# Performance work log

Hardware: AMD Instinct MI355X
Metric: run time of the kernel (lower is better)

The kernel has to match this reference:

```python
import jax, jax.numpy as jnp
import numpy as np

N_DRUG = 20000
N_DIS = 40000
E = 500000
D_IN = 128
D_OUT = 128
SLOPE = 0.01  # F.leaky_relu default negative_slope


def setup_inputs() -> dict:
    key = jax.random.key(0)
    ks = jax.random.split(key, 17)
    s = 1.0 / np.sqrt(D_IN)
    inp = {
        'feat_drug': jax.random.normal(ks[0], (N_DRUG, D_IN), jnp.float32),
        'feat_disease': jax.random.normal(ks[1], (N_DIS, D_IN), jnp.float32),
        'src_ind': jax.random.randint(ks[2], (E,), 0, N_DRUG, jnp.int32),
        'dst_ind': jax.random.randint(ks[3], (E,), 0, N_DIS, jnp.int32),
        'src_rev': jax.random.randint(ks[4], (E,), 0, N_DIS, jnp.int32),
        'dst_rev': jax.random.randint(ks[5], (E,), 0, N_DRUG, jnp.int32),
        'src_dd': jax.random.randint(ks[6], (E,), 0, N_DIS, jnp.int32),
        'dst_dd': jax.random.randint(ks[7], (E,), 0, N_DIS, jnp.int32),
        'W_ind': jax.random.normal(ks[8], (D_IN, D_OUT), jnp.float32) * s,
        'b_ind': jax.random.normal(ks[9], (D_OUT,), jnp.float32) * s,
        'W_rev': jax.random.normal(ks[10], (D_IN, D_OUT), jnp.float32) * s,
        'b_rev': jax.random.normal(ks[11], (D_OUT,), jnp.float32) * s,
        'W_dd': jax.random.normal(ks[12], (D_IN, D_OUT), jnp.float32) * s,
        'b_dd': jax.random.normal(ks[13], (D_OUT,), jnp.float32) * s,
        'a_ind': jax.random.normal(ks[14], (2 * D_OUT,), jnp.float32) * s,
        'a_rev': jax.random.normal(ks[15], (2 * D_OUT,), jnp.float32) * s,
        'a_dd': jax.random.normal(ks[16], (2 * D_OUT,), jnp.float32) * s,
    }
    return inp


def _leaky(x):
    return jnp.where(x >= 0, x, SLOPE * x)


def _etype_softmax_agg(wh_src, wh_dst, src, dst, a, n_dst):
    # per-edge message gather
    m = wh_src[src]                      # [E, D_OUT]
    wd = wh_dst[dst]                     # [E, D_OUT]
    # attn_fc(concat(m, wd)) == m @ a[:D] + wd @ a[D:]
    e = _leaky(m @ a[:D_OUT] + wd @ a[D_OUT:])   # [E]
    # segment softmax over dst (per-node mailbox softmax)
    emax = jax.ops.segment_max(e, dst, num_segments=n_dst)
    ex = jnp.exp(e - emax[dst])
    denom = jax.ops.segment_sum(ex, dst, num_segments=n_dst)
    alpha = ex / denom[dst]
    # weighted scatter-sum aggregation
    return jax.ops.segment_sum(alpha[:, None] * m, dst, num_segments=n_dst)


def reference(feat_drug, feat_disease, src_ind, dst_ind, src_rev, dst_rev,
              src_dd, dst_dd, W_ind, b_ind, W_rev, b_rev, W_dd, b_dd,
              a_ind, a_rev, a_dd):
    # per-etype linear projections of the source node type
    Wh_ind = feat_drug @ W_ind + b_ind       # drug nodes, etype 'indication'
    Wh_rev = feat_disease @ W_rev + b_rev    # disease nodes, etype 'rev_indication'
    Wh_dd = feat_disease @ W_dd + b_dd       # disease nodes, etype 'dd' (self type)
    # indication: drug->disease pairs with dst key Wh_rev_indication
    h_dis = _etype_softmax_agg(Wh_ind, Wh_rev, src_ind, dst_ind, a_ind, N_DIS)
    # dd: same src/dst type, uses Wh_dd on both sides; cross-etype 'sum' reducer
    h_dis = h_dis + _etype_softmax_agg(Wh_dd, Wh_dd, src_dd, dst_dd, a_dd, N_DIS)
    # rev_indication: disease->drug pairs with dst key Wh_indication
    h_drug = _etype_softmax_agg(Wh_rev, Wh_ind, src_rev, dst_rev, a_rev, N_DRUG)
    return (h_drug, h_dis)
```

## Files before the change

kernel.cpp:

```cpp
#include <hip/hip_runtime.h>
#include <hip/hip_bf16.h>

#define N_DRUG 20000
#define N_DIS  40000
#define NE     500000
#define D      128
#define PITCH  136
#define NTOT   100000
#define NQ     (NE / 4)
#define NQ3    (3 * NQ)
#define CSTR   16
#define WSZ    (128 * PITCH)
#define BIN    64

typedef __hip_bfloat16 bf16;
typedef __attribute__((ext_vector_type(8))) short short8;
typedef __attribute__((ext_vector_type(4))) float floatx4;

__device__ __forceinline__ float b2f(bf16 x) { return __bfloat162float(x); }

#define GB_DRUG 313
#define GB_DIS  625
#define GB_ALL  (GB_DRUG + 2 * GB_DIS)
#define GH      ((NQ3 + 255) / 256)

__global__ void k_prep(const float* __restrict__ W_ind, const float* __restrict__ W_rev,
                       const float* __restrict__ W_dd, bf16* __restrict__ WbfT)
{
    const int et = blockIdx.x >> 4;
    const int sl = blockIdx.x & 15;
    const float* W = (et == 0) ? W_ind : (et == 1) ? W_rev : W_dd;
    bf16* out = WbfT + (size_t)et * WSZ;
    int idx = sl * 1024 + threadIdx.x;
#pragma unroll
    for (int r = 0; r < 4; ++r, idx += 256) {
        int k = idx >> 7, n = idx & 127;
        out[n * PITCH + k] = __float2bfloat16(W[idx]);
    }
}

__global__ void k_gh(const float* __restrict__ feat_drug, const float* __restrict__ feat_dis,
                     const bf16* __restrict__ WbfT,
                     const float* __restrict__ b_ind, const float* __restrict__ b_rev,
                     const float* __restrict__ b_dd,
                     const float* __restrict__ a_ind, const float* __restrict__ a_rev,
                     const float* __restrict__ a_dd,
                     bf16* __restrict__ Wh_ind, bf16* __restrict__ Wh_rev,
                     bf16* __restrict__ Wh_dd,
                     float* __restrict__ s_src_ind, float* __restrict__ s_dst_rev,
                     float* __restrict__ s_src_rev, float* __restrict__ s_dst_ind,
                     float* __restrict__ s_src_dd,  float* __restrict__ s_dst_dd,
                     const int4* __restrict__ se_ind, const int4* __restrict__ d_ind,
                     const int4* __restrict__ se_dd,  const int4* __restrict__ d_dd,
                     const int4* __restrict__ se_rev, const int4* __restrict__ d_rev,
                     int* __restrict__ cnt, unsigned short* __restrict__ col)
{
    __shared__ __align__(16) bf16 WT[128 * PITCH];
    __shared__ __align__(16) bf16 FS[64 * PITCH];
    const int tid = threadIdx.x;
    const int blk = blockIdx.x;

    int gemm_blk;
    if (blk < 2 * GH) {
        if (blk & 1) {
            const int i = (blk >> 1) * 256 + tid;
            if (i >= NQ3) return;
            int4 d, s; int boff;
            if (i < NQ)          { d = d_ind[i];              s = se_ind[i];          boff = 0; }
            else if (i < 2 * NQ) { int j = i - NQ;     d = d_dd[j];  s = se_dd[j];  boff = 40000; }
            else                 { int j = i - 2 * NQ; d = d_rev[j]; s = se_rev[j]; boff = 80000; }
            int x0 = boff + d.x, x1 = boff + d.y, x2 = boff + d.z, x3 = boff + d.w;
            int r0 = atomicAdd(&cnt[x0 * CSTR], 1);
            if (r0 < BIN) col[(size_t)x0 * BIN + r0] = (unsigned short)s.x;
            int r1 = atomicAdd(&cnt[x1 * CSTR], 1);
            if (r1 < BIN) col[(size_t)x1 * BIN + r1] = (unsigned short)s.y;
            int r2 = atomicAdd(&cnt[x2 * CSTR], 1);
            if (r2 < BIN) col[(size_t)x2 * BIN + r2] = (unsigned short)s.z;
            int r3 = atomicAdd(&cnt[x3 * CSTR], 1);
            if (r3 < BIN) col[(size_t)x3 * BIN + r3] = (unsigned short)s.w;
            return;
        }
        gemm_blk = blk >> 1;
    } else {
        gemm_blk = GH + (blk - 2 * GH);
    }

    const float *feat, *bias, *a1, *a2;
    const bf16* Wt;
    bf16* Wh; float *s1, *s2;
    int M, row0;
    if (gemm_blk < GB_DRUG) {
        feat = feat_drug; M = N_DRUG; row0 = gemm_blk * 64;
        Wt = WbfT; bias = b_ind; a1 = a_ind; a2 = a_rev + D;
        Wh = Wh_ind; s1 = s_src_ind; s2 = s_dst_rev;
    } else if (gemm_blk < GB_DRUG + GB_DIS) {
        feat = feat_dis; M = N_DIS; row0 = (gemm_blk - GB_DRUG) * 64;
        Wt = WbfT + WSZ; bias = b_rev; a1 = a_rev; a2 = a_ind + D;
        Wh = Wh_rev; s1 = s_src_rev; s2 = s_dst_ind;
    } else {
        feat = feat_dis; M = N_DIS; row0 = (gemm_blk - GB_DRUG - GB_DIS) * 64;
        Wt = WbfT + 2 * WSZ; bias = b_dd; a1 = a_dd; a2 = a_dd + D;
        Wh = Wh_dd; s1 = s_src_dd; s2 = s_dst_dd;
    }

#pragma unroll
    for (int rep = 0; rep < 9; ++rep) {
        int off = rep * 2048 + tid * 8;
        if (off < WSZ)
            *(short8*)(WT + off) = *(const short8*)(Wt + off);
    }
#pragma unroll
    for (int rep = 0; rep < 8; ++rep) {
        int idx = rep * 1024 + tid * 4;
        int r = idx >> 7, k = idx & 127;
        int gr = row0 + r;
        float4 f4 = (gr < M) ? *(const float4*)(feat + (size_t)gr * D + k)
                             : make_float4(0.f, 0.f, 0.f, 0.f);
        FS[r * PITCH + k + 0] = __float2bfloat16(f4.x);
        FS[r * PITCH + k + 1] = __float2bfloat16(f4.y);
        FS[r * PITCH + k + 2] = __float2bfloat16(f4.z);
        FS[r * PITCH + k + 3] = __float2bfloat16(f4.w);
    }
    __syncthreads();

    const int wave = tid >> 6;
    const int lane = tid & 63;
    const int m0   = wave * 16;
    const int arow = lane & 15;
    const int kq   = lane >> 4;

    floatx4 acc[8];
#pragma unroll
    for (int t = 0; t < 8; ++t) acc[t] = (floatx4){0.f, 0.f, 0.f, 0.f};

#pragma unroll
    for (int ks = 0; ks < 4; ++ks) {
        const int kb = ks * 32 + kq * 8;
        short8 afrag = *(const short8*)(FS + (m0 + arow) * PITCH + kb);
#pragma unroll
        for (int t = 0; t < 8; ++t) {
            short8 bfrag = *(const short8*)(WT + (t * 16 + arow) * PITCH + kb);
            acc[t] = __builtin_amdgcn_mfma_f32_16x16x32_bf16(afrag, bfrag, acc[t], 0, 0, 0);
        }
    }

    const int crow = m0 + kq * 4;
    float p1[4] = {0.f, 0.f, 0.f, 0.f};
    float p2[4] = {0.f, 0.f, 0.f, 0.f};
#pragma unroll
    for (int t = 0; t < 8; ++t) {
        const int n = t * 16 + arow;
        const float bn = bias[n], a1n = a1[n], a2n = a2[n];
#pragma unroll
        for (int r = 0; r < 4; ++r) {
            float v = acc[t][r] + bn;
            int gr = row0 + crow + r;
            if (gr < M) Wh[(size_t)gr * D + n] = __float2bfloat16(v);
            p1[r] += v * a1n;
            p2[r] += v * a2n;
        }
    }
#pragma unroll
    for (int r = 0; r < 4; ++r) {
#pragma unroll
        for (int off = 1; off < 16; off <<= 1) {
            p1[r] += __shfl_xor(p1[r], off);
            p2[r] += __shfl_xor(p2[r], off);
        }
    }
    if (arow == 0) {
#pragma unroll
        for (int r = 0; r < 4; ++r) {
            int gr = row0 + crow + r;
            if (gr < M) { s1[gr] = p1[r]; s2[gr] = p2[r]; }
        }
    }
}

__device__ __forceinline__ float2 agg_seg(int b, int c, const unsigned short* __restrict__ col,
                                          const float* __restrict__ ssrc, float sdv,
                                          const bf16* __restrict__ Whs, int lane)
{
    float ax = 0.f, ay = 0.f, dpart = 0.f;
    for (int t0 = 0; t0 < c; t0 += 64) {
        const int rem = c - t0;
        const int k = rem < 64 ? rem : 64;
        int myc = 0; float myex = 0.f;
        if (lane < k) {
            myc = col[b + t0 + lane];
            float e = ssrc[myc] + sdv;
            e = (e >= 0.f) ? e : 0.01f * e;
            myex = __expf(fminf(e, 30.f));
        }
        dpart += myex;
        const int kk = (k + 7) & ~7;
        for (int j = 0; j < kk; j += 8) {
            int sv[8]; float ev[8]; __hip_bfloat162 w[8];
#pragma unroll
            for (int u = 0; u < 8; ++u) {
                sv[u] = __shfl(myc, j + u);
                ev[u] = __shfl(myex, j + u);
            }
#pragma unroll
            for (int u = 0; u < 8; ++u)
                w[u] = *(const __hip_bfloat162*)(Whs + (size_t)sv[u] * D + 2 * lane);
#pragma unroll
            for (int u = 0; u < 8; ++u) {
                ax += ev[u] * b2f(w[u].x);
                ay += ev[u] * b2f(w[u].y);
            }
        }
    }
    float denom = dpart;
#pragma unroll
    for (int off = 32; off; off >>= 1) denom += __shfl_xor(denom, off);
    const float inv = (c > 0) ? 1.f / denom : 0.f;
    return make_float2(ax * inv, ay * inv);
}

__global__ void k_agg(const int* __restrict__ cnt, const unsigned short* __restrict__ col,
                      const float* __restrict__ ss_ind, const float* __restrict__ sd_ind,
                      const bf16* __restrict__ Wh_ind,
                      const float* __restrict__ ss_dd, const float* __restrict__ sd_dd,
                      const bf16* __restrict__ Wh_dd,
                      const float* __restrict__ ss_rev, const float* __restrict__ sd_rev,
                      const bf16* __restrict__ Wh_rev,
                      float* __restrict__ out_dis, float* __restrict__ out_drug)
{
    const int g    = (int)((blockIdx.x * blockDim.x + threadIdx.x) >> 6);
    const int lane = threadIdx.x & 63;
    if (g < N_DIS) {
        float2 r1 = agg_seg(g * BIN, cnt[g * CSTR], col,
                            ss_ind, sd_ind[g], Wh_ind, lane);
        float2 r2 = agg_seg((40000 + g) * BIN, cnt[(40000 + g) * CSTR], col,
                            ss_dd, sd_dd[g], Wh_dd, lane);
        *(float2*)(out_dis + (size_t)g * D + 2 * lane) = make_float2(r1.x + r2.x, r1.y + r2.y);
    } else if (g < N_DIS + N_DRUG) {
        const int gg = g - N_DIS;
        float2 r = agg_seg((80000 + gg) * BIN, cnt[(80000 + gg) * CSTR], col,
                           ss_rev, sd_rev[gg], Wh_rev, lane);
        *(float2*)(out_drug + (size_t)gg * D + 2 * lane) = r;
    }
}

extern "C" void kernel_launch(void* const* d_in, const int* in_sizes, int n_in,
                              void* d_out, int out_size, void* d_ws, size_t ws_size,
                              hipStream_t stream)
{
    const float* feat_drug = (const float*)d_in[0];
    const float* feat_dis  = (const float*)d_in[1];
    const int*   src_ind   = (const int*)d_in[2];
    const int*   dst_ind   = (const int*)d_in[3];
    const int*   src_rev   = (const int*)d_in[4];
    const int*   dst_rev   = (const int*)d_in[5];
    const int*   src_dd    = (const int*)d_in[6];
    const int*   dst_dd    = (const int*)d_in[7];
    const float* W_ind     = (const float*)d_in[8];
    const float* b_ind     = (const float*)d_in[9];
    const float* W_rev     = (const float*)d_in[10];
    const float* b_rev     = (const float*)d_in[11];
    const float* W_dd      = (const float*)d_in[12];
    const float* b_dd      = (const float*)d_in[13];
    const float* a_ind     = (const float*)d_in[14];
    const float* a_rev     = (const float*)d_in[15];
    const float* a_dd      = (const float*)d_in[16];

    float* out_drug = (float*)d_out;
    float* out_dis  = (float*)d_out + (size_t)N_DRUG * D;

    char* ws = (char*)d_ws;
    size_t off = 0;
    auto alloc = [&](size_t bytes) -> void* {
        void* p = ws + off;
        off += (bytes + 255) & ~(size_t)255;
        return p;
    };

    bf16* Wh_ind = (bf16*)alloc(sizeof(bf16) * (size_t)N_DRUG * D);
    bf16* Wh_rev = (bf16*)alloc(sizeof(bf16) * (size_t)N_DIS * D);
    bf16* Wh_dd  = (bf16*)alloc(sizeof(bf16) * (size_t)N_DIS * D);
    bf16* WbfT   = (bf16*)alloc(sizeof(bf16) * 3 * WSZ);

    float* s_src_ind = (float*)alloc(sizeof(float) * N_DRUG);
    float* s_dst_rev = (float*)alloc(sizeof(float) * N_DRUG);
    float* s_src_rev = (float*)alloc(sizeof(float) * N_DIS);
    float* s_dst_ind = (float*)alloc(sizeof(float) * N_DIS);
    float* s_src_dd  = (float*)alloc(sizeof(float) * N_DIS);
    float* s_dst_dd  = (float*)alloc(sizeof(float) * N_DIS);

    unsigned short* col = (unsigned short*)alloc(sizeof(unsigned short) * (size_t)NTOT * BIN);

    const size_t nzero = (size_t)NTOT * CSTR;
    int* cnt = (int*)alloc(sizeof(int) * nzero);

    hipMemsetAsync(cnt, 0, sizeof(int) * nzero, stream);

    k_prep<<<48, 256, 0, stream>>>(W_ind, W_rev, W_dd, WbfT);

    k_gh<<<GB_ALL + GH, 256, 0, stream>>>(
        feat_drug, feat_dis, WbfT, b_ind, b_rev, b_dd,
        a_ind, a_rev, a_dd, Wh_ind, Wh_rev, Wh_dd,
        s_src_ind, s_dst_rev, s_src_rev, s_dst_ind, s_src_dd, s_dst_dd,
        (const int4*)src_ind, (const int4*)dst_ind,
        (const int4*)src_dd,  (const int4*)dst_dd,
        (const int4*)src_rev, (const int4*)dst_rev,
        cnt, col);

    k_agg<<<(N_DIS + N_DRUG + 3) / 4, 256, 0, stream>>>(cnt, col,
                                                        s_src_ind, s_dst_ind, Wh_ind,
                                                        s_src_dd, s_dst_dd, Wh_dd,
                                                        s_src_rev, s_dst_rev, Wh_rev,
                                                        out_dis, out_drug);
}
```

Baseline: 234.8 us.

## Fuse memset into prep kernel and interleave two disease segment aggregations

Replaces the separate hipMemsetAsync with zeroing done by extra blocks inside the weight-prep kernel, removing one launch. In the aggregation kernel, the indication and dd segments for each disease node are now processed together in one loop, issuing both sets of gathered row loads before accumulating, so more memory requests are in flight per wavefront. Counts are clamped to BIN, which also guards against overflowing the column bins. This costs more registers per thread, which may lower occupancy.

```diff
diff --git a/kernel.cpp b/kernel.cpp
--- a/kernel.cpp
+++ b/kernel.cpp
@@ -12,6 +12,7 @@
 #define CSTR   16
 #define WSZ    (128 * PITCH)
 #define BIN    64
+#define NZERO4 ((NTOT * CSTR) / 4)
 
 typedef __hip_bfloat16 bf16;
 typedef __attribute__((ext_vector_type(8))) short short8;
@@ -24,18 +25,26 @@
 #define GB_ALL  (GB_DRUG + 2 * GB_DIS)
 #define GH      ((NQ3 + 255) / 256)
 
-__global__ void k_prep(const float* __restrict__ W_ind, const float* __restrict__ W_rev,
-                       const float* __restrict__ W_dd, bf16* __restrict__ WbfT)
-{
-    const int et = blockIdx.x >> 4;
-    const int sl = blockIdx.x & 15;
-    const float* W = (et == 0) ? W_ind : (et == 1) ? W_rev : W_dd;
-    bf16* out = WbfT + (size_t)et * WSZ;
-    int idx = sl * 1024 + threadIdx.x;
-#pragma unroll
-    for (int r = 0; r < 4; ++r, idx += 256) {
-        int k = idx >> 7, n = idx & 127;
-        out[n * PITCH + k] = __float2bfloat16(W[idx]);
+__global__ void k_init(const float* __restrict__ W_ind, const float* __restrict__ W_rev,
+                       const float* __restrict__ W_dd, bf16* __restrict__ WbfT,
+                       int4* __restrict__ zr4)
+{
+    const int blk = blockIdx.x;
+    if (blk < 48) {
+        const int et = blk >> 4;
+        const int sl = blk & 15;
+        const float* W = (et == 0) ? W_ind : (et == 1) ? W_rev : W_dd;
+        bf16* out = WbfT + (size_t)et * WSZ;
+        int idx = sl * 1024 + threadIdx.x;
+#pragma unroll
+        for (int r = 0; r < 4; ++r, idx += 256) {
+            int k = idx >> 7, n = idx & 127;
+            out[n * PITCH + k] = __float2bfloat16(W[idx]);
+        }
+    } else {
+        const int4 z = make_int4(0, 0, 0, 0);
+        for (int j = (blk - 48) * 256 + threadIdx.x; j < NZERO4; j += 400 * 256)
+            zr4[j] = z;
     }
 }
 
@@ -230,15 +239,84 @@
     const int g    = (int)((blockIdx.x * blockDim.x + threadIdx.x) >> 6);
     const int lane = threadIdx.x & 63;
     if (g < N_DIS) {
-        float2 r1 = agg_seg(g * BIN, cnt[g * CSTR], col,
-                            ss_ind, sd_ind[g], Wh_ind, lane);
-        float2 r2 = agg_seg((40000 + g) * BIN, cnt[(40000 + g) * CSTR], col,
-                            ss_dd, sd_dd[g], Wh_dd, lane);
-        *(float2*)(out_dis + (size_t)g * D + 2 * lane) = make_float2(r1.x + r2.x, r1.y + r2.y);
+        int cA = cnt[g * CSTR];             cA = cA < BIN ? cA : BIN;
+        int cB = cnt[(40000 + g) * CSTR];   cB = cB < BIN ? cB : BIN;
+        const size_t bA = (size_t)g * BIN;
+        const size_t bB = (size_t)(40000 + g) * BIN;
+        int mycA = 0, mycB = 0; float exA = 0.f, exB = 0.f;
+        if (lane < cA) {
+            mycA = col[bA + lane];
+            float e = ss_ind[mycA] + sd_ind[g];
+            e = (e >= 0.f) ? e : 0.01f * e;
+            exA = __expf(fminf(e, 30.f));
+        }
+        if (lane < cB) {
+            mycB = col[bB + lane];
+            float e = ss_dd[mycB] + sd_dd[g];
+            e = (e >= 0.f) ? e : 0.01f * e;
+            exB = __expf(fminf(e, 30.f));
+        }
+        float dA = exA, dB = exB;
+#pragma unroll
+        for (int off = 32; off; off >>= 1) {
+            dA += __shfl_xor(dA, off);
+            dB += __shfl_xor(dB, off);
+        }
+        float ax = 0.f, ay = 0.f, bx = 0.f, by = 0.f;
+        const int kkA = (cA + 7) & ~7;
+        const int kkB = (cB + 7) & ~7;
+        const int kkM = kkA > kkB ? kkA : kkB;
+        for (int j = 0; j < kkM; j += 8) {
+            const bool doA = j < kkA, doB = j < kkB;
+            int svA[8], svB[8]; float evA[8], evB[8];
+            __hip_bfloat162 wA[8], wB[8];
+            if (doA) {
+#pragma unroll
+                for (int u = 0; u < 8; ++u) {
+                    svA[u] = __shfl(mycA, j + u);
+                    evA[u] = __shfl(exA, j + u);
+                }
+            }
+            if (doB) {
+#pragma unroll
+                for (int u = 0; u < 8; ++u) {
+                    svB[u] = __shfl(mycB, j + u);
+                    evB[u] = __shfl(exB, j + u);
+                }
+            }
+            if (doA) {
+#pragma unroll
+                for (int u = 0; u < 8; ++u)
+                    wA[u] = *(const __hip_bfloat162*)(Wh_ind + (size_t)svA[u] * D + 2 * lane);
+            }
+            if (doB) {
+#pragma unroll
+                for (int u = 0; u < 8; ++u)
+                    wB[u] = *(const __hip_bfloat162*)(Wh_dd + (size_t)svB[u] * D + 2 * lane);
+            }
+            if (doA) {
+#pragma unroll
+                for (int u = 0; u < 8; ++u) {
+                    ax += evA[u] * b2f(wA[u].x);
+                    ay += evA[u] * b2f(wA[u].y);
+                }
+            }
+            if (doB) {
+#pragma unroll
+                for (int u = 0; u < 8; ++u) {
+                    bx += evB[u] * b2f(wB[u].x);
+                    by += evB[u] * b2f(wB[u].y);
+                }
+            }
+        }
+        const float invA = (cA > 0) ? 1.f / dA : 0.f;
+        const float invB = (cB > 0) ? 1.f / dB : 0.f;
+        *(float2*)(out_dis + (size_t)g * D + 2 * lane) =
+            make_float2(ax * invA + bx * invB, ay * invA + by * invB);
     } else if (g < N_DIS + N_DRUG) {
         const int gg = g - N_DIS;
-        float2 r = agg_seg((80000 + gg) * BIN, cnt[(80000 + gg) * CSTR], col,
-                           ss_rev, sd_rev[gg], Wh_rev, lane);
+        int c = cnt[(80000 + gg) * CSTR]; c = c < BIN ? c : BIN;
+        float2 r = agg_seg((80000 + gg) * BIN, c, col, ss_rev, sd_rev[gg], Wh_rev, lane);
         *(float2*)(out_drug + (size_t)gg * D + 2 * lane) = r;
     }
 }
@@ -293,9 +371,7 @@
     const size_t nzero = (size_t)NTOT * CSTR;
     int* cnt = (int*)alloc(sizeof(int) * nzero);
 
-    hipMemsetAsync(cnt, 0, sizeof(int) * nzero, stream);
-
-    k_prep<<<48, 256, 0, stream>>>(W_ind, W_rev, W_dd, WbfT);
+    k_init<<<448, 256, 0, stream>>>(W_ind, W_rev, W_dd, WbfT, (int4*)cnt);
 
     k_gh<<<GB_ALL + GH, 256, 0, stream>>>(
         feat_drug, feat_dis, WbfT, b_ind, b_rev, b_dd,
```

Measured after the change: 247.0 us. 1.05x slower.
